# Kernel tuning notes

Measured on AMD Instinct MI355X. Metric: run time of the kernel, lower is better.

## Reference

```python
import jax, jax.numpy as jnp
import numpy as np

DIM = 2048
MEM = 64
EPS = 1e-5


def setup_inputs() -> dict:
    key = jax.random.key(0)
    ks = jax.random.split(key, 6)
    x = jax.random.normal(ks[0], (8, 4096, DIM), dtype=jnp.float32)
    memory_slots = jax.random.normal(ks[1], (MEM, DIM), dtype=jnp.float32) * 0.02
    # memory_gate: Linear(dim -> memory_size)
    Wg = jax.random.normal(ks[2], (DIM, MEM), dtype=jnp.float32) / np.sqrt(DIM)
    bg = jnp.zeros((MEM,), dtype=jnp.float32)
    # memory_update: Linear(2*dim -> dim)
    Wu = jax.random.normal(ks[3], (2 * DIM, DIM), dtype=jnp.float32) / np.sqrt(2 * DIM)
    bu = jnp.zeros((DIM,), dtype=jnp.float32)
    gamma = jnp.ones((DIM,), dtype=jnp.float32)
    beta = jnp.zeros((DIM,), dtype=jnp.float32)
    return {"x": x, "memory_slots": memory_slots, "Wg": Wg, "bg": bg,
            "Wu": Wu, "bu": bu, "gamma": gamma, "beta": beta}


def _layer_norm(h, gamma, beta):
    mu = jnp.mean(h, axis=-1, keepdims=True)
    var = jnp.mean(jnp.square(h - mu), axis=-1, keepdims=True)
    return (h - mu) * jax.lax.rsqrt(var + EPS) * gamma + beta


def reference(x, memory_slots, Wg, bg, Wu, bu, gamma, beta):
    # gates: [B, S, M]
    memory_gates = jax.nn.sigmoid(jnp.einsum('bsd,dm->bsm', x, Wg) + bg)
    # retrieval: [B, S, D]
    memory_retrieved = jnp.einsum('bsm,md->bsd', memory_gates, memory_slots)
    combined = jnp.concatenate([x, memory_retrieved], axis=-1)  # [B, S, 2D]
    memory_enhanced = jnp.einsum('bse,ed->bsd', combined, Wu) + bu
    return _layer_norm(memory_enhanced, gamma, beta)
```

## Files before the change

kernel.cpp:

```cpp
#include <hip/hip_runtime.h>
#include <hip/hip_bf16.h>

typedef __bf16 bf16x8 __attribute__((ext_vector_type(8)));
typedef float f32x4 __attribute__((ext_vector_type(4)));
typedef float f32x16 __attribute__((ext_vector_type(16)));
typedef unsigned short u16;
typedef u16 u16x8 __attribute__((ext_vector_type(8)));

#define DIM 2048
#define MEM 64
#define KC 2112
#define MTOK 32768
#define BK 32
#define NT (KC/BK)

__device__ __forceinline__ u16 f2bf(float f) {
  union { float f; unsigned u; } v; v.f = f;
  unsigned r = v.u + 0x7FFF + ((v.u >> 16) & 1);
  return (u16)(r >> 16);
}

#define GLDS16(g, l) __builtin_amdgcn_global_load_lds( \
    (const __attribute__((address_space(1))) void*)(g), \
    (__attribute__((address_space(3))) void*)(l), 16, 0, 0)

__global__ __launch_bounds__(256) void prep_wu1(const float* __restrict__ Wu,
                                                u16* __restrict__ WcatT) {
  __shared__ float tile[64][65];
  int bk = blockIdx.x & 31;
  int bn = blockIdx.x >> 5;
  int tx = threadIdx.x & 63, g = threadIdx.x >> 6;
#pragma unroll
  for (int i = 0; i < 16; ++i)
    tile[g + i*4][tx] = Wu[(size_t)(bk*64 + g + i*4)*DIM + bn*64 + tx];
  __syncthreads();
#pragma unroll
  for (int i = 0; i < 16; ++i) {
    int n = bn*64 + g + i*4;
    WcatT[(size_t)n*KC + bk*64 + tx] = f2bf(tile[tx][g + i*4]);
  }
}

__global__ __launch_bounds__(256) void prep_m2a(const float* __restrict__ ms,
                                                const float* __restrict__ Wu,
                                                float* __restrict__ M2p) {
  int n  = blockIdx.x*256 + threadIdx.x;
  int mg = blockIdx.y;
  int kc = blockIdx.z;
  const float* w2 = Wu + (size_t)DIM*DIM + n;
  const float* m0 = ms + (size_t)(mg*4+0)*DIM;
  const float* m1 = ms + (size_t)(mg*4+1)*DIM;
  const float* m2 = ms + (size_t)(mg*4+2)*DIM;
  const float* m3 = ms + (size_t)(mg*4+3)*DIM;
  float a0=0.f, a1=0.f, a2=0.f, a3=0.f;
  int d0 = kc*256;
  for (int d = d0; d < d0+256; ++d) {
    float w = w2[(size_t)d*DIM];
    a0 += m0[d]*w; a1 += m1[d]*w; a2 += m2[d]*w; a3 += m3[d]*w;
  }
  M2p[((size_t)kc*64 + mg*4 + 0)*2048 + n] = a0;
  M2p[((size_t)kc*64 + mg*4 + 1)*2048 + n] = a1;
  M2p[((size_t)kc*64 + mg*4 + 2)*2048 + n] = a2;
  M2p[((size_t)kc*64 + mg*4 + 3)*2048 + n] = a3;
}

__global__ __launch_bounds__(256) void prep_m2b(const float* __restrict__ M2p,
                                                u16* __restrict__ WcatT) {
  int i = blockIdx.x*256 + threadIdx.x;
  float s = 0.f;
#pragma unroll
  for (int kc = 0; kc < 8; ++kc) s += M2p[(size_t)kc*131072 + i];
  int m = i >> 11, n = i & 2047;
  WcatT[(size_t)n*KC + DIM + m] = f2bf(s);
}

__global__ __launch_bounds__(256) void prep_wg(const float* __restrict__ Wg,
                                               u16* __restrict__ WgT) {
  __shared__ float tile[64][65];
  int k0 = blockIdx.x * 64;
  int tx = threadIdx.x & 63, g = threadIdx.x >> 6;
#pragma unroll
  for (int i = 0; i < 16; ++i)
    tile[g + i*4][tx] = Wg[(size_t)(k0 + g + i*4)*MEM + tx];
  __syncthreads();
#pragma unroll
  for (int i = 0; i < 16; ++i) {
    int m = g + i*4;
    WgT[(size_t)m*DIM + k0 + tx] = f2bf(tile[tx][m]);
  }
}

__global__ __launch_bounds__(256) void conv_x(const float* __restrict__ x,
                                              u16* __restrict__ Acat) {
  size_t i = ((size_t)blockIdx.x*256 + threadIdx.x) * 8;
  size_t t = i >> 11;
  int c = (int)(i & 2047);
  const float4* p = reinterpret_cast<const float4*>(x + i);
  float4 a = p[0], b = p[1];
  u16x8 o;
  o[0]=f2bf(a.x); o[1]=f2bf(a.y); o[2]=f2bf(a.z); o[3]=f2bf(a.w);
  o[4]=f2bf(b.x); o[5]=f2bf(b.y); o[6]=f2bf(b.z); o[7]=f2bf(b.w);
  *reinterpret_cast<u16x8*>(Acat + t*KC + c) = o;
}

__global__ __launch_bounds__(256) void gates_gemm(const u16* __restrict__ Acat,
                                                  const u16* __restrict__ WgT,
                                                  const float* __restrict__ bg,
                                                  u16* __restrict__ Aout) {
  __shared__ u16 As[128*32];
  __shared__ u16 Bs[64*32];
  int brow = blockIdx.x;
  int tid = threadIdx.x;
  int w = tid >> 6, l = tid & 63;
  int lrow = l & 15, lk = l >> 4;

  const u16* Ag  = Acat + (size_t)(brow*128 + (tid>>2))*KC + (tid&3)*8;
  const u16* Ag2 = Acat + (size_t)(brow*128 + 64 + (tid>>2))*KC + (tid&3)*8;
  const u16* Bg  = WgT  + (size_t)(tid>>2)*DIM + (tid&3)*8;
  u16* Asd  = As + tid*8;
  u16* Asd2 = As + 2048 + tid*8;
  u16* Bsd  = Bs + tid*8;

  f32x4 acc[2][4] = {};
  const bf16x8* Al = reinterpret_cast<const bf16x8*>(As);
  const bf16x8* Bl = reinterpret_cast<const bf16x8*>(Bs);
  int abase = (w*32 + lrow)*4 + lk;
  int bbase = lrow*4 + lk;

  for (int k0 = 0; k0 < DIM; k0 += 32) {
    GLDS16(Ag, Asd); GLDS16(Ag2, Asd2); GLDS16(Bg, Bsd);
    Ag += 32; Ag2 += 32; Bg += 32;
    __syncthreads();
    bf16x8 av[2], bv[4];
#pragma unroll
    for (int m = 0; m < 2; ++m) av[m] = Al[abase + m*64];
#pragma unroll
    for (int n = 0; n < 4; ++n) bv[n] = Bl[bbase + n*64];
#pragma unroll
    for (int m = 0; m < 2; ++m)
#pragma unroll
      for (int n = 0; n < 4; ++n)
        acc[m][n] = __builtin_amdgcn_mfma_f32_16x16x32_bf16(av[m], bv[n], acc[m][n], 0, 0, 0);
    __syncthreads();
  }

#pragma unroll
  for (int n = 0; n < 4; ++n) {
    int c = n*16 + lrow;
    float b = bg[c];
#pragma unroll
    for (int m = 0; m < 2; ++m)
#pragma unroll
      for (int r = 0; r < 4; ++r) {
        int t = brow*128 + w*32 + m*16 + lk*4 + r;
        float logit = acc[m][n][r] + b;
        float gv = 1.0f / (1.0f + __expf(-logit));
        Aout[(size_t)t*KC + DIM + c] = f2bf(gv);
      }
  }
}

__global__ __launch_bounds__(512, 2) void gemm_main8(const u16* __restrict__ A,
                                                     const u16* __restrict__ Bt,
                                                     const float* __restrict__ bu,
                                                     float* __restrict__ H) {
  __shared__ u16 AsB[4*8192];
  __shared__ u16 BsB[4*8192];

  const int bid = blockIdx.x;
  const int wg  = (bid & 7) * (int)(gridDim.x >> 3) + (bid >> 3);
  const int brow = wg >> 3;
  const int bcol = wg & 7;
  const int tid = threadIdx.x;
  const int w = tid >> 6, l = tid & 63;
  const int wm = w >> 2, wn = w & 3;
  const int l31 = l & 31, lr5 = l >> 5;

  const int xor5  = ((tid >> 5) & 1) << 5;
  const int kelem = (((tid & 3) * 16) ^ xor5) >> 1;
  const int rowst = tid >> 2;
  const u16* Asrc0 = A  + (size_t)(brow*256 + rowst)*KC + kelem;
  const u16* Asrc1 = A  + (size_t)(brow*256 + 128 + rowst)*KC + kelem;
  const u16* Bsrc0 = Bt + (size_t)(bcol*256 + rowst)*KC + kelem;
  const u16* Bsrc1 = Bt + (size_t)(bcol*256 + 128 + rowst)*KC + kelem;
  const int p0 = tid*16, p1 = 8192 + tid*16;
  char* AsC = (char*)AsB;
  char* BsC = (char*)BsB;

  int aoff[4][2], boff[2][2];
#pragma unroll
  for (int rf = 0; rf < 4; ++rf)
#pragma unroll
    for (int ks = 0; ks < 2; ++ks) {
      int row = wm*128 + rf*32 + l31;
      int lg  = row*64 + ks*32 + lr5*16;
      aoff[rf][ks] = lg ^ (((row >> 3) & 1) << 5);
    }
#pragma unroll
  for (int cf = 0; cf < 2; ++cf)
#pragma unroll
    for (int ks = 0; ks < 2; ++ks) {
      int row = wn*64 + cf*32 + l31;
      int lg  = row*64 + ks*32 + lr5*16;
      boff[cf][ks] = lg ^ (((row >> 3) & 1) << 5);
    }

  f32x16 acc[4][2] = {};

#define STAGE_A(kt) { const int bb_ = ((kt)&3)*16384; \
    GLDS16(Asrc0 + (size_t)(kt)*BK, AsC + bb_ + p0); \
    GLDS16(Asrc1 + (size_t)(kt)*BK, AsC + bb_ + p1); }
#define STAGE_B(kt) { const int bb_ = ((kt)&3)*16384; \
    GLDS16(Bsrc0 + (size_t)(kt)*BK, BsC + bb_ + p0); \
    GLDS16(Bsrc1 + (size_t)(kt)*BK, BsC + bb_ + p1); }
#define MFMA32(av, bv, c) __builtin_amdgcn_mfma_f32_32x32x16_bf16(av, bv, c, 0, 0, 0)

  STAGE_A(0); STAGE_B(0);
  STAGE_A(1); STAGE_B(1);
  STAGE_A(2); STAGE_B(2);
  asm volatile("s_waitcnt vmcnt(8)" ::: "memory");
  __builtin_amdgcn_sched_barrier(0);
  __builtin_amdgcn_s_barrier();

#pragma unroll 1
  for (int t = 0; t < NT; ++t) {
    const char* Ab = AsC + (t & 3) * 16384;
    const char* Bb = BsC + (t & 3) * 16384;

    bf16x8 b00 = *(const bf16x8*)(Bb + boff[0][0]);
    bf16x8 b01 = *(const bf16x8*)(Bb + boff[0][1]);
    bf16x8 b10 = *(const bf16x8*)(Bb + boff[1][0]);
    bf16x8 b11 = *(const bf16x8*)(Bb + boff[1][1]);
    bf16x8 a00 = *(const bf16x8*)(Ab + aoff[0][0]);
    bf16x8 a01 = *(const bf16x8*)(Ab + aoff[0][1]);
    bf16x8 a10 = *(const bf16x8*)(Ab + aoff[1][0]);
    bf16x8 a11 = *(const bf16x8*)(Ab + aoff[1][1]);
    if (t + 3 < NT) STAGE_A(t + 3);
    __builtin_amdgcn_s_barrier();
    asm volatile("s_waitcnt lgkmcnt(0)" ::: "memory");
    __builtin_amdgcn_sched_barrier(0);
    __builtin_amdgcn_s_setprio(1);
    acc[0][0] = MFMA32(a00, b00, acc[0][0]);
    acc[0][1] = MFMA32(a00, b10, acc[0][1]);
    acc[1][0] = MFMA32(a10, b00, acc[1][0]);
    acc[1][1] = MFMA32(a10, b10, acc[1][1]);
    acc[0][0] = MFMA32(a01, b01, acc[0][0]);
    acc[0][1] = MFMA32(a01, b11, acc[0][1]);
    acc[1][0] = MFMA32(a11, b01, acc[1][0]);
    acc[1][1] = MFMA32(a11, b11, acc[1][1]);
    __builtin_amdgcn_s_setprio(0);
    __builtin_amdgcn_s_barrier();

    bf16x8 a20 = *(const bf16x8*)(Ab + aoff[2][0]);
    bf16x8 a21 = *(const bf16x8*)(Ab + aoff[2][1]);
    bf16x8 a30 = *(const bf16x8*)(Ab + aoff[3][0]);
    bf16x8 a31 = *(const bf16x8*)(Ab + aoff[3][1]);
    if (t + 3 < NT) STAGE_B(t + 3);
    __builtin_amdgcn_s_barrier();
    asm volatile("s_waitcnt lgkmcnt(0)" ::: "memory");
    __builtin_amdgcn_sched_barrier(0);
    __builtin_amdgcn_s_setprio(1);
    acc[2][0] = MFMA32(a20, b00, acc[2][0]);
    acc[2][1] = MFMA32(a20, b10, acc[2][1]);
    acc[3][0] = MFMA32(a30, b00, acc[3][0]);
    acc[3][1] = MFMA32(a30, b10, acc[3][1]);
    acc[2][0] = MFMA32(a21, b01, acc[2][0]);
    acc[2][1] = MFMA32(a21, b11, acc[2][1]);
    acc[3][0] = MFMA32(a31, b01, acc[3][0]);
    acc[3][1] = MFMA32(a31, b11, acc[3][1]);
    __builtin_amdgcn_s_setprio(0);
    if (t <= NT-4)      { asm volatile("s_waitcnt vmcnt(8)" ::: "memory"); }
    else if (t == NT-3) { asm volatile("s_waitcnt vmcnt(4)" ::: "memory"); }
    else                { asm volatile("s_waitcnt vmcnt(0)" ::: "memory"); }
    __builtin_amdgcn_sched_barrier(0);
    __builtin_amdgcn_s_barrier();
  }
#undef STAGE_A
#undef STAGE_B
#undef MFMA32

  const int orow = brow*256 + wm*128;
  const int ocol = bcol*256 + wn*64;
#pragma unroll
  for (int cf = 0; cf < 2; ++cf) {
    const int c = ocol + cf*32 + l31;
    const float bias = bu[c];
#pragma unroll
    for (int rf = 0; rf < 4; ++rf) {
      const int br = orow + rf*32 + 4*lr5;
#pragma unroll
      for (int reg = 0; reg < 16; ++reg) {
        const int row = br + (reg & 3) + 8*(reg >> 2);
        H[(size_t)row*DIM + c] = acc[rf][cf][reg] + bias;
      }
    }
  }
}

__global__ __launch_bounds__(256) void ln_inplace(float* __restrict__ H,
                                                  const float* __restrict__ gamma,
                                                  const float* __restrict__ beta) {
  int row = blockIdx.x;
  float* h = H + (size_t)row*DIM;
  int tid = threadIdx.x;
  float4 a = reinterpret_cast<const float4*>(h)[tid*2];
  float4 b = reinterpret_cast<const float4*>(h)[tid*2+1];
  float v[8] = {a.x,a.y,a.z,a.w,b.x,b.y,b.z,b.w};
  float s = 0.f, s2 = 0.f;
#pragma unroll
  for (int j = 0; j < 8; ++j) { s += v[j]; s2 += v[j]*v[j]; }
#pragma unroll
  for (int o = 32; o >= 1; o >>= 1) { s += __shfl_xor(s, o); s2 += __shfl_xor(s2, o); }
  __shared__ float ss[4], ss2[4];
  int w = tid >> 6;
  if ((tid & 63) == 0) { ss[w] = s; ss2[w] = s2; }
  __syncthreads();
  s  = ss[0]+ss[1]+ss[2]+ss[3];
  s2 = ss2[0]+ss2[1]+ss2[2]+ss2[3];
  float mu  = s * (1.0f/DIM);
  float var = s2 * (1.0f/DIM) - mu*mu;
  float rs  = rsqrtf(var + 1e-5f);
  int c0 = tid*8;
  float o8[8];
#pragma unroll
  for (int j = 0; j < 8; ++j) o8[j] = (v[j]-mu)*rs*gamma[c0+j] + beta[c0+j];
  float4 oa = {o8[0],o8[1],o8[2],o8[3]}, ob = {o8[4],o8[5],o8[6],o8[7]};
  reinterpret_cast<float4*>(h)[tid*2]   = oa;
  reinterpret_cast<float4*>(h)[tid*2+1] = ob;
}

extern "C" void kernel_launch(void* const* d_in, const int* in_sizes, int n_in,
                              void* d_out, int out_size, void* d_ws, size_t ws_size,
                              hipStream_t stream) {
  const float* x     = (const float*)d_in[0];
  const float* ms    = (const float*)d_in[1];
  const float* Wg    = (const float*)d_in[2];
  const float* bg    = (const float*)d_in[3];
  const float* Wu    = (const float*)d_in[4];
  const float* bu    = (const float*)d_in[5];
  const float* gamma = (const float*)d_in[6];
  const float* beta  = (const float*)d_in[7];
  float* out = (float*)d_out;

  char* wsp = (char*)d_ws;
  u16* Acat  = (u16*)wsp;
  u16* WcatT = (u16*)(wsp + (size_t)MTOK*KC*2);
  u16* WgT   = (u16*)(wsp + (size_t)MTOK*KC*2 + (size_t)DIM*KC*2);
  float* M2p = (float*)wsp;

  prep_m2a<<<dim3(8,16,8), 256, 0, stream>>>(ms, Wu, M2p);
  prep_m2b<<<512, 256, 0, stream>>>(M2p, WcatT);
  prep_wu1<<<1024, 256, 0, stream>>>(Wu, WcatT);
  prep_wg<<<32, 256, 0, stream>>>(Wg, WgT);
  conv_x<<<32768, 256, 0, stream>>>(x, Acat);
  gates_gemm<<<256, 256, 0, stream>>>(Acat, WgT, bg, Acat);
  gemm_main8<<<1024, 512, 0, stream>>>(Acat, WcatT, bu, out);
  ln_inplace<<<32768, 256, 0, stream>>>(out, gamma, beta);
}
```

Baseline: 578.6 us.

## Store pre-norm GEMM output as bf16 and restructure MFMA loop barriers

The main GEMM's pre-LayerNorm output is written to a bf16 workspace buffer when the workspace is large enough. A new LayerNorm kernel reads that buffer and writes fp32 output, which halves the intermediate write and read traffic. The K-loop is also reordered: each half-iteration now uses one k-slice across all four A fragments, and the intra-iteration barriers and lgkmcnt waits are removed, which cuts synchronisation. Rounding the intermediate to bf16 before normalisation adds precision error, and without the explicit waits the compiler must insert correct LDS waits itself.

```diff
diff --git a/kernel.cpp b/kernel.cpp
--- a/kernel.cpp
+++ b/kernel.cpp
@@ -18,6 +18,9 @@
   union { float f; unsigned u; } v; v.f = f;
   unsigned r = v.u + 0x7FFF + ((v.u >> 16) & 1);
   return (u16)(r >> 16);
+}
+__device__ __forceinline__ float bf2f(u16 u) {
+  union { unsigned u; float f; } v; v.u = ((unsigned)u) << 16; return v.f;
 }
 
 #define GLDS16(g, l) __builtin_amdgcn_global_load_lds( \
@@ -163,7 +166,8 @@
 __global__ __launch_bounds__(512, 2) void gemm_main8(const u16* __restrict__ A,
                                                      const u16* __restrict__ Bt,
                                                      const float* __restrict__ bu,
-                                                     float* __restrict__ H) {
+                                                     float* __restrict__ Hf,
+                                                     u16* __restrict__ Hb) {
   __shared__ u16 AsB[4*8192];
   __shared__ u16 BsB[4*8192];
 
@@ -221,59 +225,55 @@
   asm volatile("s_waitcnt vmcnt(8)" ::: "memory");
   __builtin_amdgcn_sched_barrier(0);
   __builtin_amdgcn_s_barrier();
+  __builtin_amdgcn_sched_barrier(0);
 
 #pragma unroll 1
   for (int t = 0; t < NT; ++t) {
     const char* Ab = AsC + (t & 3) * 16384;
     const char* Bb = BsC + (t & 3) * 16384;
 
-    bf16x8 b00 = *(const bf16x8*)(Bb + boff[0][0]);
-    bf16x8 b01 = *(const bf16x8*)(Bb + boff[0][1]);
-    bf16x8 b10 = *(const bf16x8*)(Bb + boff[1][0]);
-    bf16x8 b11 = *(const bf16x8*)(Bb + boff[1][1]);
-    bf16x8 a00 = *(const bf16x8*)(Ab + aoff[0][0]);
-    bf16x8 a01 = *(const bf16x8*)(Ab + aoff[0][1]);
-    bf16x8 a10 = *(const bf16x8*)(Ab + aoff[1][0]);
-    bf16x8 a11 = *(const bf16x8*)(Ab + aoff[1][1]);
+    bf16x8 a0 = *(const bf16x8*)(Ab + aoff[0][0]);
+    bf16x8 a1 = *(const bf16x8*)(Ab + aoff[1][0]);
+    bf16x8 a2 = *(const bf16x8*)(Ab + aoff[2][0]);
+    bf16x8 a3 = *(const bf16x8*)(Ab + aoff[3][0]);
+    bf16x8 b0 = *(const bf16x8*)(Bb + boff[0][0]);
+    bf16x8 b1 = *(const bf16x8*)(Bb + boff[1][0]);
     if (t + 3 < NT) STAGE_A(t + 3);
-    __builtin_amdgcn_s_barrier();
-    asm volatile("s_waitcnt lgkmcnt(0)" ::: "memory");
-    __builtin_amdgcn_sched_barrier(0);
     __builtin_amdgcn_s_setprio(1);
-    acc[0][0] = MFMA32(a00, b00, acc[0][0]);
-    acc[0][1] = MFMA32(a00, b10, acc[0][1]);
-    acc[1][0] = MFMA32(a10, b00, acc[1][0]);
-    acc[1][1] = MFMA32(a10, b10, acc[1][1]);
-    acc[0][0] = MFMA32(a01, b01, acc[0][0]);
-    acc[0][1] = MFMA32(a01, b11, acc[0][1]);
-    acc[1][0] = MFMA32(a11, b01, acc[1][0]);
-    acc[1][1] = MFMA32(a11, b11, acc[1][1]);
+    acc[0][0] = MFMA32(a0, b0, acc[0][0]);
+    acc[0][1] = MFMA32(a0, b1, acc[0][1]);
+    acc[1][0] = MFMA32(a1, b0, acc[1][0]);
+    acc[1][1] = MFMA32(a1, b1, acc[1][1]);
+    acc[2][0] = MFMA32(a2, b0, acc[2][0]);
+    acc[2][1] = MFMA32(a2, b1, acc[2][1]);
+    acc[3][0] = MFMA32(a3, b0, acc[3][0]);
+    acc[3][1] = MFMA32(a3, b1, acc[3][1]);
     __builtin_amdgcn_s_setprio(0);
-    __builtin_amdgcn_s_barrier();
-
-    bf16x8 a20 = *(const bf16x8*)(Ab + aoff[2][0]);
-    bf16x8 a21 = *(const bf16x8*)(Ab + aoff[2][1]);
-    bf16x8 a30 = *(const bf16x8*)(Ab + aoff[3][0]);
-    bf16x8 a31 = *(const bf16x8*)(Ab + aoff[3][1]);
+
+    bf16x8 a4 = *(const bf16x8*)(Ab + aoff[0][1]);
+    bf16x8 a5 = *(const bf16x8*)(Ab + aoff[1][1]);
+    bf16x8 a6 = *(const bf16x8*)(Ab + aoff[2][1]);
+    bf16x8 a7 = *(const bf16x8*)(Ab + aoff[3][1]);
+    bf16x8 b2 = *(const bf16x8*)(Bb + boff[0][1]);
+    bf16x8 b3 = *(const bf16x8*)(Bb + boff[1][1]);
     if (t + 3 < NT) STAGE_B(t + 3);
-    __builtin_amdgcn_s_barrier();
-    asm volatile("s_waitcnt lgkmcnt(0)" ::: "memory");
-    __builtin_amdgcn_sched_barrier(0);
     __builtin_amdgcn_s_setprio(1);
-    acc[2][0] = MFMA32(a20, b00, acc[2][0]);
-    acc[2][1] = MFMA32(a20, b10, acc[2][1]);
-    acc[3][0] = MFMA32(a30, b00, acc[3][0]);
-    acc[3][1] = MFMA32(a30, b10, acc[3][1]);
-    acc[2][0] = MFMA32(a21, b01, acc[2][0]);
-    acc[2][1] = MFMA32(a21, b11, acc[2][1]);
-    acc[3][0] = MFMA32(a31, b01, acc[3][0]);
-    acc[3][1] = MFMA32(a31, b11, acc[3][1]);
+    acc[0][0] = MFMA32(a4, b2, acc[0][0]);
+    acc[0][1] = MFMA32(a4, b3, acc[0][1]);
+    acc[1][0] = MFMA32(a5, b2, acc[1][0]);
+    acc[1][1] = MFMA32(a5, b3, acc[1][1]);
+    acc[2][0] = MFMA32(a6, b2, acc[2][0]);
+    acc[2][1] = MFMA32(a6, b3, acc[2][1]);
+    acc[3][0] = MFMA32(a7, b2, acc[3][0]);
+    acc[3][1] = MFMA32(a7, b3, acc[3][1]);
     __builtin_amdgcn_s_setprio(0);
+
     if (t <= NT-4)      { asm volatile("s_waitcnt vmcnt(8)" ::: "memory"); }
     else if (t == NT-3) { asm volatile("s_waitcnt vmcnt(4)" ::: "memory"); }
     else                { asm volatile("s_waitcnt vmcnt(0)" ::: "memory"); }
     __builtin_amdgcn_sched_barrier(0);
     __builtin_amdgcn_s_barrier();
+    __builtin_amdgcn_sched_barrier(0);
   }
 #undef STAGE_A
 #undef STAGE_B
@@ -281,31 +281,50 @@
 
   const int orow = brow*256 + wm*128;
   const int ocol = bcol*256 + wn*64;
-#pragma unroll
-  for (int cf = 0; cf < 2; ++cf) {
-    const int c = ocol + cf*32 + l31;
-    const float bias = bu[c];
-#pragma unroll
-    for (int rf = 0; rf < 4; ++rf) {
-      const int br = orow + rf*32 + 4*lr5;
-#pragma unroll
-      for (int reg = 0; reg < 16; ++reg) {
-        const int row = br + (reg & 3) + 8*(reg >> 2);
-        H[(size_t)row*DIM + c] = acc[rf][cf][reg] + bias;
+  if (Hb) {
+#pragma unroll
+    for (int cf = 0; cf < 2; ++cf) {
+      const int c = ocol + cf*32 + l31;
+      const float bias = bu[c];
+#pragma unroll
+      for (int rf = 0; rf < 4; ++rf) {
+        const int br = orow + rf*32 + 4*lr5;
+#pragma unroll
+        for (int reg = 0; reg < 16; ++reg) {
+          const int row = br + (reg & 3) + 8*(reg >> 2);
+          Hb[(size_t)row*DIM + c] = f2bf(acc[rf][cf][reg] + bias);
+        }
       }
     }
-  }
-}
-
-__global__ __launch_bounds__(256) void ln_inplace(float* __restrict__ H,
-                                                  const float* __restrict__ gamma,
-                                                  const float* __restrict__ beta) {
+  } else {
+#pragma unroll
+    for (int cf = 0; cf < 2; ++cf) {
+      const int c = ocol + cf*32 + l31;
+      const float bias = bu[c];
+#pragma unroll
+      for (int rf = 0; rf < 4; ++rf) {
+        const int br = orow + rf*32 + 4*lr5;
+#pragma unroll
+        for (int reg = 0; reg < 16; ++reg) {
+          const int row = br + (reg & 3) + 8*(reg >> 2);
+          Hf[(size_t)row*DIM + c] = acc[rf][cf][reg] + bias;
+        }
+      }
+    }
+  }
+}
+
+__global__ __launch_bounds__(256) void ln_b(const u16* __restrict__ Hb,
+                                            float* __restrict__ out,
+                                            const float* __restrict__ gamma,
+                                            const float* __restrict__ beta) {
   int row = blockIdx.x;
-  float* h = H + (size_t)row*DIM;
+  const u16* h = Hb + (size_t)row*DIM;
   int tid = threadIdx.x;
-  float4 a = reinterpret_cast<const float4*>(h)[tid*2];
-  float4 b = reinterpret_cast<const float4*>(h)[tid*2+1];
-  float v[8] = {a.x,a.y,a.z,a.w,b.x,b.y,b.z,b.w};
+  u16x8 hv = *reinterpret_cast<const u16x8*>(h + tid*8);
+  float v[8];
+#pragma unroll
+  for (int j = 0; j < 8; ++j) v[j] = bf2f(hv[j]);
   float s = 0.f, s2 = 0.f;
 #pragma unroll
   for (int j = 0; j < 8; ++j) { s += v[j]; s2 += v[j]*v[j]; }
@@ -325,6 +344,39 @@
 #pragma unroll
   for (int j = 0; j < 8; ++j) o8[j] = (v[j]-mu)*rs*gamma[c0+j] + beta[c0+j];
   float4 oa = {o8[0],o8[1],o8[2],o8[3]}, ob = {o8[4],o8[5],o8[6],o8[7]};
+  float* op = out + (size_t)row*DIM;
+  reinterpret_cast<float4*>(op)[tid*2]   = oa;
+  reinterpret_cast<float4*>(op)[tid*2+1] = ob;
+}
+
+__global__ __launch_bounds__(256) void ln_inplace(float* __restrict__ H,
+                                                  const float* __restrict__ gamma,
+                                                  const float* __restrict__ beta) {
+  int row = blockIdx.x;
+  float* h = H + (size_t)row*DIM;
+  int tid = threadIdx.x;
+  float4 a = reinterpret_cast<const float4*>(h)[tid*2];
+  float4 b = reinterpret_cast<const float4*>(h)[tid*2+1];
+  float v[8] = {a.x,a.y,a.z,a.w,b.x,b.y,b.z,b.w};
+  float s = 0.f, s2 = 0.f;
+#pragma unroll
+  for (int j = 0; j < 8; ++j) { s += v[j]; s2 += v[j]*v[j]; }
+#pragma unroll
+  for (int o = 32; o >= 1; o >>= 1) { s += __shfl_xor(s, o); s2 += __shfl_xor(s2, o); }
+  __shared__ float ss[4], ss2[4];
+  int w = tid >> 6;
+  if ((tid & 63) == 0) { ss[w] = s; ss2[w] = s2; }
+  __syncthreads();
+  s  = ss[0]+ss[1]+ss[2]+ss[3];
+  s2 = ss2[0]+ss2[1]+ss2[2]+ss2[3];
+  float mu  = s * (1.0f/DIM);
+  float var = s2 * (1.0f/DIM) - mu*mu;
+  float rs  = rsqrtf(var + 1e-5f);
+  int c0 = tid*8;
+  float o8[8];
+#pragma unroll
+  for (int j = 0; j < 8; ++j) o8[j] = (v[j]-mu)*rs*gamma[c0+j] + beta[c0+j];
+  float4 oa = {o8[0],o8[1],o8[2],o8[3]}, ob = {o8[4],o8[5],o8[6],o8[7]};
   reinterpret_cast<float4*>(h)[tid*2]   = oa;
   reinterpret_cast<float4*>(h)[tid*2+1] = ob;
 }
@@ -343,10 +395,17 @@
   float* out = (float*)d_out;
 
   char* wsp = (char*)d_ws;
-  u16* Acat  = (u16*)wsp;
-  u16* WcatT = (u16*)(wsp + (size_t)MTOK*KC*2);
-  u16* WgT   = (u16*)(wsp + (size_t)MTOK*KC*2 + (size_t)DIM*KC*2);
+  const size_t offAcat  = 0;
+  const size_t offWcatT = offAcat  + (size_t)MTOK*KC*2;
+  const size_t offWgT   = offWcatT + (size_t)DIM*KC*2;
+  const size_t offHb    = offWgT   + (size_t)MEM*DIM*2;
+  const size_t needHb   = offHb + (size_t)MTOK*DIM*2;
+
+  u16* Acat  = (u16*)(wsp + offAcat);
+  u16* WcatT = (u16*)(wsp + offWcatT);
+  u16* WgT   = (u16*)(wsp + offWgT);
   float* M2p = (float*)wsp;
+  u16* Hb    = (ws_size >= needHb) ? (u16*)(wsp + offHb) : nullptr;
 
   prep_m2a<<<dim3(8,16,8), 256, 0, stream>>>(ms, Wu, M2p);
   prep_m2b<<<512, 256, 0, stream>>>(M2p, WcatT);
@@ -354,6 +413,7 @@
   prep_wg<<<32, 256, 0, stream>>>(Wg, WgT);
   conv_x<<<32768, 256, 0, stream>>>(x, Acat);
   gates_gemm<<<256, 256, 0, stream>>>(Acat, WgT, bg, Acat);
-  gemm_main8<<<1024, 512, 0, stream>>>(Acat, WcatT, bu, out);
-  ln_inplace<<<32768, 256, 0, stream>>>(out, gamma, beta);
-}
+  gemm_main8<<<1024, 512, 0, stream>>>(Acat, WcatT, bu, out, Hb);
+  if (Hb) ln_b<<<32768, 256, 0, stream>>>(Hb, out, gamma, beta);
+  else    ln_inplace<<<32768, 256, 0, stream>>>(out, gamma, beta);
+}
```

Result: faster. 513.2 us (-11.3%).
